# Performance work log

Hardware: AMD Instinct MI355X
Metric: run time of the kernel (lower is better)

Reference implementation:

```python
import jax, jax.numpy as jnp
import numpy as np

B, L, E, H = 4, 512, 2048, 32
S = E // H  # head_size = 64
EXTRA_MAA, EXTRA_DECAY = 32, 64
EPS = 1e-5


def setup_inputs() -> dict:
    key = jax.random.key(0)
    ks = jax.random.split(key, 24)
    rn = lambda k, shp, s=1.0: jax.random.normal(k, shp, dtype=jnp.float32) * s
    return dict(
        x=rn(ks[0], (B, L, E)),
        state=rn(ks[1], (B, 2 + S, E), 0.1),
        ln1_w=jnp.ones((E,), jnp.float32), ln1_b=jnp.zeros((E,), jnp.float32),
        ln2_w=jnp.ones((E,), jnp.float32), ln2_b=jnp.zeros((E,), jnp.float32),
        maa_x=rn(ks[2], (E,), 0.02),
        maa_w1=rn(ks[3], (E, 5 * EXTRA_MAA), 0.02),
        maa_w2=rn(ks[4], (5, EXTRA_MAA, E), 0.02),
        maa_stack=rn(ks[5], (5, E), 0.02),          # [k,w,v,r,g] time_maa vectors
        time_decay=rn(ks[6], (E,), 0.5),
        decay_w1=rn(ks[7], (E, EXTRA_DECAY), 0.02),
        decay_w2=rn(ks[8], (EXTRA_DECAY, E), 0.02),
        faaaa=rn(ks[9], (H, S), 0.1),
        Wr=rn(ks[10], (E, E), 0.02), Wk=rn(ks[11], (E, E), 0.02),
        Wv=rn(ks[12], (E, E), 0.02), Wg=rn(ks[13], (E, E), 0.02),
        Wo=rn(ks[14], (E, E), 0.02),
        gn_w=jnp.ones((E,), jnp.float32), gn_b=jnp.zeros((E,), jnp.float32),
        ffn_maa_k=rn(ks[15], (E,), 0.02), ffn_maa_r=rn(ks[16], (E,), 0.02),
        ffn_Wk=rn(ks[17], (E, E), 0.02), ffn_Wr=rn(ks[18], (E, E), 0.02),
        ffn_Wv=rn(ks[19], (E, E), 0.02),
        i=0,
    )


def _ln(x, w, b):
    m = jnp.mean(x, axis=-1, keepdims=True)
    v = jnp.mean((x - m) ** 2, axis=-1, keepdims=True)
    return (x - m) * jax.lax.rsqrt(v + EPS) * w + b


def _token_shift(xn, prev_row):
    # sx_lerp[t] = x[t-1] - x[t], with state row as x[-1]
    first = (prev_row - xn[:, 0])[:, None]
    rest = xn[:, :-1] - xn[:, 1:]
    return jnp.concatenate([first, rest], axis=1)


def reference(x, state, ln1_w, ln1_b, ln2_w, ln2_b, maa_x, maa_w1, maa_w2,
              maa_stack, time_decay, decay_w1, decay_w2, faaaa,
              Wr, Wk, Wv, Wg, Wo, gn_w, gn_b,
              ffn_maa_k, ffn_maa_r, ffn_Wk, ffn_Wr, ffn_Wv, i):
    b, l = x.shape[0], x.shape[1]
    i0 = (2 + S) * i + 0
    i1 = (2 + S) * i + 1

    # ---- time mixing (parallel) ----
    xn = _ln(x, ln1_w, ln1_b)
    sx = _token_shift(xn, state[:, i1])
    xxx = jnp.tanh((xn + sx * maa_x) @ maa_w1).reshape(b, l, 5, 1, EXTRA_MAA)
    xxx = jnp.matmul(xxx, maa_w2).reshape(b, l, 5, E)   # [B,L,5,E]
    x5 = xn[:, :, None] + sx[:, :, None] * (maa_stack + xxx)

    w = jnp.exp(-jnp.exp(time_decay + jnp.tanh(x5[:, :, 1] @ decay_w1) @ decay_w2))
    w = w.reshape(b, l, H, S)
    r = (x5[:, :, 3] @ Wr.T).reshape(b, l, H, S)
    k = (x5[:, :, 0] @ Wk.T).reshape(b, l, H, S)
    v = (x5[:, :, 2] @ Wv.T).reshape(b, l, H, S)
    g = jax.nn.silu(x5[:, :, 4] @ Wg.T)                 # [B,L,E]

    s0 = state[:, (2 + S) * i + 2:(2 + S) * (i + 1)].reshape(b, H, S, S)
    u = faaaa[None, :, :, None]                         # [1,H,S,1]

    def step(s, rkvw):
        r_t, k_t, v_t, w_t = rkvw                      # each [B,H,S]
        a = k_t[:, :, :, None] * v_t[:, :, None, :]    # [B,H,S,S] outer product
        out = jnp.einsum('bhk,bhkd->bhd', r_t, u * a + s)
        return a + w_t[:, :, :, None] * s, out

    xs = tuple(jnp.moveaxis(t, 1, 0) for t in (r, k, v, w))
    _, outs = jax.lax.scan(step, s0, xs)               # outs [L,B,H,S]
    att = jnp.moveaxis(outs, 0, 1).reshape(b, l, E)

    # group norm over each head's channels
    a4 = att.reshape(b, l, H, S)
    m = jnp.mean(a4, axis=-1, keepdims=True)
    var = jnp.mean((a4 - m) ** 2, axis=-1, keepdims=True)
    att = ((a4 - m) * jax.lax.rsqrt(var + EPS)).reshape(b, l, E) * gn_w + gn_b
    x = x + (att * g) @ Wo.T

    # ---- channel mixing (parallel) ----
    xn2 = _ln(x, ln2_w, ln2_b)
    sx2 = _token_shift(xn2, state[:, i0])
    xk = xn2 + sx2 * ffn_maa_k
    xr = xn2 + sx2 * ffn_maa_r
    rr = jax.nn.sigmoid(xr @ ffn_Wr.T)
    kk = jnp.square(jax.nn.relu(xk @ ffn_Wk.T))
    x = x + rr * (kk @ ffn_Wv.T)
    return x
```

## Files before the change

kernel.cpp:

```cpp
#include <hip/hip_runtime.h>

#define EE 2048
#define LL 512
#define BBATCH 4
#define HH 32
#define SS 64
#define EPSF 1e-5f
static constexpr size_t NEL = (size_t)BBATCH * LL * EE;

typedef __attribute__((ext_vector_type(8))) short short8;
typedef __attribute__((ext_vector_type(4))) float f32x4;

__device__ __forceinline__ unsigned short f2bf(float f) {
  union { float f; unsigned u; } x; x.f = f;
  return (unsigned short)((x.u + 0x7fffu + ((x.u >> 16) & 1u)) >> 16);
}

__device__ __forceinline__ void gload_lds16(const unsigned short* g, unsigned short* l) {
  __builtin_amdgcn_global_load_lds((const __attribute__((address_space(1))) void*)g,
                                   (__attribute__((address_space(3))) void*)l, 16, 0, 0);
}

struct CvArgs {
  const float* s[4];
  unsigned short* d[4];
};
__global__ void __launch_bounds__(256) f2bf_batch(CvArgs a, int n4) {
  int z = blockIdx.y;
  int idx = blockIdx.x * 256 + threadIdx.x;
  if (idx >= n4) return;
  float4 v = ((const float4*)a.s[z])[idx];
  ushort4 o;
  o.x = f2bf(v.x); o.y = f2bf(v.y); o.z = f2bf(v.z); o.w = f2bf(v.w);
  ((ushort4*)a.d[z])[idx] = o;
}

__global__ void __launch_bounds__(256) wprep_kernel(const float* __restrict__ w1,
                                                    const float* __restrict__ w2,
                                                    const float* __restrict__ d1,
                                                    const float* __restrict__ d2,
                                                    unsigned short* __restrict__ w1T,
                                                    unsigned short* __restrict__ w2cat,
                                                    unsigned short* __restrict__ dw1T,
                                                    unsigned short* __restrict__ dw2T) {
  const int N0 = 256 * 2048;
  const int N1 = 10240 * 160;
  const int N2 = 128 * 2048;
  const int N3 = 2048 * 128;
  int id = blockIdx.x * 256 + threadIdx.x;
  if (id < N0) {
    int n = id >> 11, k = id & 2047;
    float v = (n < 160) ? w1[(size_t)k * 160 + n] : 0.f;
    w1T[id] = f2bf(v);
    return;
  }
  id -= N0;
  if (id < N1) {
    int n = id / 160, kq = id - n * 160;
    int j = n >> 11, e = n & 2047;
    float v = ((kq >> 5) == j) ? w2[(size_t)kq * 2048 + e] : 0.f;
    w2cat[id] = f2bf(v);
    return;
  }
  id -= N1;
  if (id < N2) {
    int n = id >> 11, k = id & 2047;
    float v = (n < 64) ? d1[(size_t)k * 64 + n] : 0.f;
    dw1T[id] = f2bf(v);
    return;
  }
  id -= N2;
  if (id < N3) {
    int n = id >> 7, k = id & 127;
    float v = (k < 64) ? d2[(size_t)k * 2048 + n] : 0.f;
    dw2T[id] = f2bf(v);
  }
}

__global__ void __launch_bounds__(256) ln_kernel(const float* __restrict__ x,
                                                 const float* __restrict__ wt,
                                                 const float* __restrict__ bs,
                                                 float* __restrict__ out) {
  __shared__ float red[4];
  int tid = threadIdx.x;
  size_t base = (size_t)blockIdx.x * EE;
  int e = tid * 8;
  float4 v0 = *(const float4*)&x[base + e];
  float4 v1 = *(const float4*)&x[base + e + 4];
  float s = v0.x + v0.y + v0.z + v0.w + v1.x + v1.y + v1.z + v1.w;
#pragma unroll
  for (int off = 32; off >= 1; off >>= 1) s += __shfl_xor(s, off);
  if ((tid & 63) == 0) red[tid >> 6] = s;
  __syncthreads();
  float mean = (red[0] + red[1] + red[2] + red[3]) * (1.f / EE);
  __syncthreads();
  float d, q = 0.f;
  d = v0.x - mean; q += d * d; d = v0.y - mean; q += d * d;
  d = v0.z - mean; q += d * d; d = v0.w - mean; q += d * d;
  d = v1.x - mean; q += d * d; d = v1.y - mean; q += d * d;
  d = v1.z - mean; q += d * d; d = v1.w - mean; q += d * d;
#pragma unroll
  for (int off = 32; off >= 1; off >>= 1) q += __shfl_xor(q, off);
  if ((tid & 63) == 0) red[tid >> 6] = q;
  __syncthreads();
  float var = (red[0] + red[1] + red[2] + red[3]) * (1.f / EE);
  float rstd = rsqrtf(var + EPSF);
  float4 w0 = *(const float4*)&wt[e], w1 = *(const float4*)&wt[e + 4];
  float4 b0 = *(const float4*)&bs[e], b1 = *(const float4*)&bs[e + 4];
  float4 o0, o1;
  o0.x = (v0.x - mean) * rstd * w0.x + b0.x;
  o0.y = (v0.y - mean) * rstd * w0.y + b0.y;
  o0.z = (v0.z - mean) * rstd * w0.z + b0.z;
  o0.w = (v0.w - mean) * rstd * w0.w + b0.w;
  o1.x = (v1.x - mean) * rstd * w1.x + b1.x;
  o1.y = (v1.y - mean) * rstd * w1.y + b1.y;
  o1.z = (v1.z - mean) * rstd * w1.z + b1.z;
  o1.w = (v1.w - mean) * rstd * w1.w + b1.w;
  *(float4*)&out[base + e] = o0;
  *(float4*)&out[base + e + 4] = o1;
}

__global__ void __launch_bounds__(256) shift_kernel(const float* __restrict__ xn,
                                                    const float* __restrict__ state,
                                                    const int* __restrict__ ip,
                                                    const float* __restrict__ maa_x,
                                                    unsigned short* __restrict__ xxm,
                                                    float* __restrict__ sx) {
  int tok = blockIdx.x;
  int b = tok >> 9, t = tok & 511;
  int tid = threadIdx.x;
  const float* cur = xn + (size_t)tok * EE;
  const float* prev = (t == 0)
      ? (state + ((size_t)b * (2 + SS) + (size_t)(2 + SS) * (*ip) + 1) * EE)
      : (cur - EE);
  int e = tid * 8;
#pragma unroll
  for (int half = 0; half < 2; ++half) {
    int eh = e + half * 4;
    float4 c = *(const float4*)&cur[eh];
    float4 p = *(const float4*)&prev[eh];
    float4 mx = *(const float4*)&maa_x[eh];
    float4 sv;
    sv.x = p.x - c.x; sv.y = p.y - c.y; sv.z = p.z - c.z; sv.w = p.w - c.w;
    *(float4*)&sx[(size_t)tok * EE + eh] = sv;
    ushort4 xo;
    xo.x = f2bf(c.x + sv.x * mx.x);
    xo.y = f2bf(c.y + sv.y * mx.y);
    xo.z = f2bf(c.z + sv.z * mx.z);
    xo.w = f2bf(c.w + sv.w * mx.w);
    *(ushort4*)&xxm[(size_t)tok * EE + eh] = xo;
  }
}

template <int BM, int BN, int BK>
__device__ __forceinline__ void gemm_core(const unsigned short* __restrict__ A, int lda,
                                          const unsigned short* __restrict__ W, int ldw,
                                          int K, int NB, unsigned short* As, unsigned short* Bs,
                                          f32x4 (&acc)[BM / 32][BN / 32], int& m0o, int& n0o) {
  constexpr int FM = BM / 32, FN = BN / 32;
  constexpr int GPR = BK / 8;
  constexpr int LA = BM * GPR / 256;
  constexpr int LB = BN * GPR / 256;
  int nwg = gridDim.x, bid = blockIdx.x;
  int qd = nwg >> 3;
  int wg = (bid & 7) * qd + (bid >> 3);
  int bm = wg / NB, bn = wg - bm * NB;
  int tid = threadIdx.x;
  int wave = tid >> 6, lane = tid & 63;
  int wm = wave >> 1, wn = wave & 1;
  const unsigned short* Abase = A + (size_t)bm * BM * lda;
  const unsigned short* Bbase = W + (size_t)bn * BN * ldw;
  for (int k0 = 0; k0 < K; k0 += BK) {
    __syncthreads();
#pragma unroll
    for (int r = 0; r < LA; ++r) {
      int g = r * 256 + tid;
      int row = g / GPR, p = g & (GPR - 1);
      int lg = p ^ (row & (GPR - 1));
      gload_lds16(Abase + (size_t)row * lda + k0 + lg * 8, &As[g * 8]);
    }
#pragma unroll
    for (int r = 0; r < LB; ++r) {
      int g = r * 256 + tid;
      int row = g / GPR, p = g & (GPR - 1);
      int lg = p ^ (row & (GPR - 1));
      gload_lds16(Bbase + (size_t)row * ldw + k0 + lg * 8, &Bs[g * 8]);
    }
    __syncthreads();
    int q = lane >> 4;
    int rA = wm * (BM / 2) + (lane & 15);
    int rB = wn * (BN / 2) + (lane & 15);
    int xrA = rA & (GPR - 1), xrB = rB & (GPR - 1);
#pragma unroll
    for (int ks = 0; ks < BK / 32; ++ks) {
      short8 av[FM], bv[FN];
#pragma unroll
      for (int f = 0; f < FM; f++) {
        int p = (ks * 4 + q) ^ xrA;
        av[f] = *(const short8*)&As[(rA + f * 16) * BK + p * 8];
      }
#pragma unroll
      for (int f = 0; f < FN; f++) {
        int p = (ks * 4 + q) ^ xrB;
        bv[f] = *(const short8*)&Bs[(rB + f * 16) * BK + p * 8];
      }
#pragma unroll
      for (int fm = 0; fm < FM; fm++)
#pragma unroll
        for (int fn = 0; fn < FN; fn++)
          acc[fm][fn] =
              __builtin_amdgcn_mfma_f32_16x16x32_bf16(av[fm], bv[fn], acc[fm][fn], 0, 0, 0);
    }
  }
  m0o = bm * BM + wm * (BM / 2);
  n0o = bn * BN + wn * (BN / 2);
}

template <int FM, int FN, typename F>
__device__ __forceinline__ void epi_loop(f32x4 (&acc)[FM][FN], int m0, int n0, F f) {
  int lane = threadIdx.x & 63;
  int rl = (lane >> 4) * 4, cl = lane & 15;
#pragma unroll
  for (int fm = 0; fm < FM; fm++)
#pragma unroll
    for (int fn = 0; fn < FN; fn++)
#pragma unroll
      for (int q = 0; q < 4; q++)
        f(m0 + fm * 16 + rl + q, n0 + fn * 16 + cl, acc[fm][fn][q]);
}

template <int MODE, int BM, int BN, int BK>
__global__ void __launch_bounds__(256) gemm_bt(const unsigned short* __restrict__ A, int lda,
                                               const unsigned short* __restrict__ W, int ldw,
                                               int K, int NB, void* __restrict__ Cout, int ldc,
                                               const float* __restrict__ p1,
                                               const float* __restrict__ p2,
                                               const float* __restrict__ p3) {
  __shared__ __align__(16) unsigned short As[BM * BK];
  __shared__ __align__(16) unsigned short Bs[BN * BK];
  f32x4 acc[BM / 32][BN / 32] = {};
  int m0, n0;
  gemm_core<BM, BN, BK>(A, lda, W, ldw, K, NB, As, Bs, acc, m0, n0);
  epi_loop(acc, m0, n0, [&](int m, int n, float val) {
    size_t o = (size_t)m * ldc + n;
    if constexpr (MODE == 2) {
      ((float*)Cout)[o] = p1[o] + val;
    } else if constexpr (MODE == 3) {
      ((float*)Cout)[o] = p1[o] + val * (1.f / (1.f + expf(-p2[o])));
    } else if constexpr (MODE == 5) {
      ((unsigned short*)Cout)[o] = f2bf(tanhf(val));
    } else if constexpr (MODE == 6) {
      ((float*)Cout)[o] = expf(-expf(p1[n] + val));
    } else {
      int j = n >> 11, e = n & 2047;
      size_t oe = (size_t)m * EE + e;
      float xv = p1[oe];
      float sv = p2[oe];
      float st = p3[(size_t)j * EE + e];
      ((unsigned short*)Cout)[(size_t)j * NEL + oe] = f2bf(xv + sv * (st + val));
    }
  });
}

struct Proj4Args {
  const unsigned short* A[4];
  const unsigned short* W[4];
  float* C[4];
};
__global__ void __launch_bounds__(256) gemm_proj4(Proj4Args args) {
  __shared__ __align__(16) unsigned short As[128 * 64];
  __shared__ __align__(16) unsigned short Bs[128 * 64];
  int z = blockIdx.y;
  f32x4 acc[4][4] = {};
  int m0, n0;
  gemm_core<128, 128, 64>(args.A[z], EE, args.W[z], EE, EE, 16, As, Bs, acc, m0, n0);
  float* C = args.C[z];
  bool silu = (z == 3);
  epi_loop(acc, m0, n0, [&](int m, int n, float val) {
    size_t o = (size_t)m * EE + n;
    C[o] = silu ? (val / (1.f + expf(-val))) : val;
  });
}

__global__ void __launch_bounds__(256) gemm_ffn2(const unsigned short* A0,
                                                 const unsigned short* A1,
                                                 const unsigned short* W0,
                                                 const unsigned short* W1, float* C0,
                                                 unsigned short* C1) {
  __shared__ __align__(16) unsigned short As[128 * 64];
  __shared__ __align__(16) unsigned short Bs[128 * 64];
  int z = blockIdx.y;
  f32x4 acc[4][4] = {};
  int m0, n0;
  gemm_core<128, 128, 64>(z ? A1 : A0, EE, z ? W1 : W0, EE, EE, 16, As, Bs, acc, m0, n0);
  epi_loop(acc, m0, n0, [&](int m, int n, float val) {
    size_t o = (size_t)m * EE + n;
    if (z == 0) {
      C0[o] = val;
    } else {
      float rv = fmaxf(val, 0.f);
      C1[o] = f2bf(rv * rv);
    }
  });
}

__global__ void __launch_bounds__(512) scan_kernel(const float* __restrict__ r,
                                                   const float* __restrict__ k,
                                                   const float* __restrict__ v,
                                                   const float* __restrict__ w,
                                                   const float* __restrict__ state,
                                                   const float* __restrict__ faaaa,
                                                   const int* __restrict__ ip,
                                                   float* __restrict__ att) {
  __shared__ float bR[2][8][32], bK[2][8][32], bW[2][8][32];
  __shared__ float bV[2][8][64];
  __shared__ float part[8][8][64];
  int blk = blockIdx.x;
  int bh = blk >> 1, kh = blk & 1;
  int b = bh >> 5, h = bh & 31;
  int tid = threadIdx.x, wv = tid >> 6, lane = tid & 63;
  int klocal = wv * 4;
  int k0w = kh * 32 + klocal;
  int ii = *ip;
  const float* sb = state + ((size_t)b * (2 + SS) + (size_t)(2 + SS) * ii + 2) * EE;
  float s_[4], u_[4];
#pragma unroll
  for (int q = 0; q < 4; ++q) {
    int kk_ = k0w + q;
    s_[q] = sb[(size_t)(2 * h + (kk_ >> 5)) * EE + (kk_ & 31) * 64 + lane];
    u_[q] = faaaa[h * 64 + kk_];
  }
  size_t base = (size_t)b * LL * EE + (size_t)h * 64;
  int c = tid;
  bool ld = c < 320;
  int lt = c / 40, r40 = c - lt * 40;
  int la = (r40 < 24) ? (r40 >> 3) : 3;
  int lcG = (r40 < 24) ? (kh * 32 + (r40 & 7) * 4) : ((r40 - 24) * 4);
  int lcL = (r40 < 24) ? ((r40 & 7) * 4) : ((r40 - 24) * 4);
  const float* lsrc = nullptr;
  if (ld) {
    const float* arr = (la == 0) ? r : (la == 1) ? k : (la == 2) ? w : v;
    lsrc = arr + base + (size_t)lt * EE + lcG;
    float4 v0 = *(const float4*)lsrc;
    if (la == 0) *(float4*)&bR[0][lt][lcL] = v0;
    else if (la == 1) *(float4*)&bK[0][lt][lcL] = v0;
    else if (la == 2) *(float4*)&bW[0][lt][lcL] = v0;
    else *(float4*)&bV[0][lt][lcL] = v0;
  }
  __syncthreads();
  for (int g = 0; g < 64; ++g) {
    int cb = g & 1;
    float4 nv;
    if (ld && g < 63) nv = *(const float4*)(lsrc + (size_t)(g + 1) * 8 * EE);
#pragma unroll
    for (int t = 0; t < 8; ++t) {
      float vv = bV[cb][t][lane];
      float acc = 0.f;
#pragma unroll
      for (int q = 0; q < 4; ++q) {
        float rk = bR[cb][t][klocal + q];
        float kk2 = bK[cb][t][klocal + q];
        float wk = bW[cb][t][klocal + q];
        float a = kk2 * vv;
        acc = fmaf(rk, fmaf(u_[q], a, s_[q]), acc);
        s_[q] = fmaf(wk, s_[q], a);
      }
      part[t][wv][lane] = acc;
    }
    if (ld && g < 63) {
      int nb = cb ^ 1;
      if (la == 0) *(float4*)&bR[nb][lt][lcL] = nv;
      else if (la == 1) *(float4*)&bK[nb][lt][lcL] = nv;
      else if (la == 2) *(float4*)&bW[nb][lt][lcL] = nv;
      else *(float4*)&bV[nb][lt][lcL] = nv;
    }
    __syncthreads();
    {
      int t = tid >> 6, d = tid & 63;
      float tot = part[t][0][d] + part[t][1][d] + part[t][2][d] + part[t][3][d] +
                  part[t][4][d] + part[t][5][d] + part[t][6][d] + part[t][7][d];
      atomicAdd(&att[base + (size_t)(g * 8 + t) * EE + d], tot);
    }
    __syncthreads();
  }
}

__global__ void __launch_bounds__(256) gn_gate_kernel(const float* __restrict__ att,
                                                      const float* __restrict__ g,
                                                      const float* __restrict__ gnw,
                                                      const float* __restrict__ gnb,
                                                      unsigned short* __restrict__ attg) {
  int tok = blockIdx.x, tid = threadIdx.x;
  int h = tid >> 3, j = tid & 7;
  size_t base = (size_t)tok * EE + h * 64 + j * 8;
  int e = h * 64 + j * 8;
  float4 a0 = *(const float4*)&att[base];
  float4 a1 = *(const float4*)&att[base + 4];
  float s = a0.x + a0.y + a0.z + a0.w + a1.x + a1.y + a1.z + a1.w;
  s += __shfl_xor(s, 1); s += __shfl_xor(s, 2); s += __shfl_xor(s, 4);
  float mean = s * (1.f / 64.f);
  float d, q = 0.f;
  d = a0.x - mean; q += d * d; d = a0.y - mean; q += d * d;
  d = a0.z - mean; q += d * d; d = a0.w - mean; q += d * d;
  d = a1.x - mean; q += d * d; d = a1.y - mean; q += d * d;
  d = a1.z - mean; q += d * d; d = a1.w - mean; q += d * d;
  q += __shfl_xor(q, 1); q += __shfl_xor(q, 2); q += __shfl_xor(q, 4);
  float rstd = rsqrtf(q * (1.f / 64.f) + EPSF);
  float4 w0 = *(const float4*)&gnw[e], w1 = *(const float4*)&gnw[e + 4];
  float4 b0 = *(const float4*)&gnb[e], b1 = *(const float4*)&gnb[e + 4];
  float4 g0 = *(const float4*)&g[base], g1 = *(const float4*)&g[base + 4];
  ushort4 o0, o1;
  o0.x = f2bf(((a0.x - mean) * rstd * w0.x + b0.x) * g0.x);
  o0.y = f2bf(((a0.y - mean) * rstd * w0.y + b0.y) * g0.y);
  o0.z = f2bf(((a0.z - mean) * rstd * w0.z + b0.z) * g0.z);
  o0.w = f2bf(((a0.w - mean) * rstd * w0.w + b0.w) * g0.w);
  o1.x = f2bf(((a1.x - mean) * rstd * w1.x + b1.x) * g1.x);
  o1.y = f2bf(((a1.y - mean) * rstd * w1.y + b1.y) * g1.y);
  o1.z = f2bf(((a1.z - mean) * rstd * w1.z + b1.z) * g1.z);
  o1.w = f2bf(((a1.w - mean) * rstd * w1.w + b1.w) * g1.w);
  *(ushort4*)&attg[base] = o0;
  *(ushort4*)&attg[base + 4] = o1;
}

__global__ void __launch_bounds__(256) ffn_shift_kernel(const float* __restrict__ xn2,
                                                        const float* __restrict__ state,
                                                        const int* __restrict__ ip,
                                                        const float* __restrict__ mk,
                                                        const float* __restrict__ mr,
                                                        unsigned short* __restrict__ xkb,
                                                        unsigned short* __restrict__ xrb) {
  size_t i4 = (size_t)blockIdx.x * 256 + threadIdx.x;
  size_t e0 = i4 * 4;
  if (e0 >= NEL) return;
  int tok = (int)(e0 >> 11);
  int c = (int)(e0 & 2047);
  int b = tok >> 9, t = tok & 511;
  float4 cur = *(const float4*)&xn2[e0];
  float4 prev;
  if (t == 0) {
    int ii = *ip;
    prev = *(const float4*)&state[((size_t)b * (2 + SS) + (size_t)(2 + SS) * ii + 0) * EE + c];
  } else {
    prev = *(const float4*)&xn2[e0 - EE];
  }
  float4 k4 = *(const float4*)&mk[c];
  float4 r4 = *(const float4*)&mr[c];
  ushort4 ko, ro;
  ko.x = f2bf(cur.x + (prev.x - cur.x) * k4.x);
  ko.y = f2bf(cur.y + (prev.y - cur.y) * k4.y);
  ko.z = f2bf(cur.z + (prev.z - cur.z) * k4.z);
  ko.w = f2bf(cur.w + (prev.w - cur.w) * k4.w);
  ro.x = f2bf(cur.x + (prev.x - cur.x) * r4.x);
  ro.y = f2bf(cur.y + (prev.y - cur.y) * r4.y);
  ro.z = f2bf(cur.z + (prev.z - cur.z) * r4.z);
  ro.w = f2bf(cur.w + (prev.w - cur.w) * r4.w);
  *(ushort4*)&xkb[e0] = ko;
  *(ushort4*)&xrb[e0] = ro;
}

extern "C" void kernel_launch(void* const* d_in, const int* in_sizes, int n_in,
                              void* d_out, int out_size, void* d_ws, size_t ws_size,
                              hipStream_t stream) {
  const float* x = (const float*)d_in[0];
  const float* state = (const float*)d_in[1];
  const float* ln1_w = (const float*)d_in[2];
  const float* ln1_b = (const float*)d_in[3];
  const float* ln2_w = (const float*)d_in[4];
  const float* ln2_b = (const float*)d_in[5];
  const float* maa_x = (const float*)d_in[6];
  const float* maa_w1 = (const float*)d_in[7];
  const float* maa_w2 = (const float*)d_in[8];
  const float* maa_stack = (const float*)d_in[9];
  const float* time_decay = (const float*)d_in[10];
  const float* decay_w1 = (const float*)d_in[11];
  const float* decay_w2 = (const float*)d_in[12];
  const float* faaaa = (const float*)d_in[13];
  const float* Wr = (const float*)d_in[14];
  const float* Wk = (const float*)d_in[15];
  const float* Wv = (const float*)d_in[16];
  const float* Wg = (const float*)d_in[17];
  const float* Wo = (const float*)d_in[18];
  const float* gn_w = (const float*)d_in[19];
  const float* gn_b = (const float*)d_in[20];
  const float* ffn_maa_k = (const float*)d_in[21];
  const float* ffn_maa_r = (const float*)d_in[22];
  const float* fWk = (const float*)d_in[23];
  const float* fWr = (const float*)d_in[24];
  const float* fWv = (const float*)d_in[25];
  const int* ip = (const int*)d_in[26];

  char* ws = (char*)d_ws;
  const size_t MB1 = 1024 * 1024;
  unsigned short* WB0 = (unsigned short*)ws;
  unsigned short* WB1 = (unsigned short*)(ws + 8 * MB1);
  float* xn = (float*)(ws + 16 * MB1);
  unsigned short* x5b = (unsigned short*)(ws + 32 * MB1);
  float* wbuf = (float*)(ws + 72 * MB1);
  float* rbuf = (float*)(ws + 88 * MB1);
  float* kbuf = (float*)(ws + 104 * MB1);
  float* vbuf = (float*)(ws + 120 * MB1);
  float* gbuf = (float*)(ws + 136 * MB1);
  char* smalls = ws + 152 * MB1;
  unsigned short* th = (unsigned short*)smalls;
  unsigned short* w1T = (unsigned short*)(smalls + 1 * MB1);
  unsigned short* w2cat = (unsigned short*)(smalls + 2 * MB1);
  unsigned short* dw1T = (unsigned short*)(smalls + 5376 * 1024);
  unsigned short* dw2T = (unsigned short*)(smalls + 5888 * 1024);
  unsigned short* dt = (unsigned short*)(smalls + 6400 * 1024);

  unsigned short* xxm = (unsigned short*)wbuf;
  float* sx = gbuf;
  float* att = xn;
  unsigned short* WB2 = (unsigned short*)xn;
  unsigned short* WB3 = WB2 + NEL;
  unsigned short* attg = x5b;
  float* xn2 = rbuf;
  unsigned short* xkb = x5b + 1 * NEL;
  unsigned short* xrb = x5b + 2 * NEL;
  unsigned short* kkb = x5b + 3 * NEL;
  unsigned short* fWkB = x5b + 4 * NEL;
  unsigned short* fWvB = (unsigned short*)kbuf;
  float* rrraw = wbuf;

  const int thr = 256;
  const int nconv = (int)(NEL / 4);

  ln_kernel<<<BBATCH * LL, thr, 0, stream>>>(x, ln1_w, ln1_b, xn);
  shift_kernel<<<BBATCH * LL, thr, 0, stream>>>(xn, state, ip, maa_x, xxm, sx);
  wprep_kernel<<<10496, thr, 0, stream>>>(maa_w1, maa_w2, decay_w1, decay_w2, w1T, w2cat,
                                          dw1T, dw2T);
  gemm_bt<5, 64, 64, 64><<<128, thr, 0, stream>>>(xxm, 2048, w1T, 2048, 2048, 4, th, 256,
                                                  nullptr, nullptr, nullptr);
  gemm_bt<7, 128, 128, 32><<<1280, thr, 0, stream>>>(th, 256, w2cat, 160, 160, 80, x5b, 0,
                                                     xn, sx, maa_stack);
  gemm_bt<5, 64, 64, 64><<<64, thr, 0, stream>>>(x5b + 1 * NEL, 2048, dw1T, 2048, 2048, 2,
                                                 dt, 128, nullptr, nullptr, nullptr);
  gemm_bt<6, 128, 128, 64><<<256, thr, 0, stream>>>(dt, 128, dw2T, 128, 128, 16, wbuf, 2048,
                                                    time_decay, nullptr, nullptr);
  {
    CvArgs ca;
    ca.s[0] = Wk; ca.d[0] = WB0;
    ca.s[1] = Wv; ca.d[1] = WB1;
    ca.s[2] = Wr; ca.d[2] = WB2;
    ca.s[3] = Wg; ca.d[3] = WB3;
    f2bf_batch<<<dim3(4096, 4), thr, 0, stream>>>(ca, nconv);
  }
  {
    Proj4Args pa;
    pa.A[0] = x5b + 0 * NEL; pa.W[0] = WB0; pa.C[0] = kbuf;
    pa.A[1] = x5b + 2 * NEL; pa.W[1] = WB1; pa.C[1] = vbuf;
    pa.A[2] = x5b + 3 * NEL; pa.W[2] = WB2; pa.C[2] = rbuf;
    pa.A[3] = x5b + 4 * NEL; pa.W[3] = WB3; pa.C[3] = gbuf;
    gemm_proj4<<<dim3(256, 4), thr, 0, stream>>>(pa);
  }
  {
    CvArgs cb;
    cb.s[0] = Wo; cb.d[0] = WB0;
    cb.s[1] = fWr; cb.d[1] = WB1;
    cb.s[2] = fWk; cb.d[2] = fWkB;
    cb.s[3] = fWk; cb.d[3] = fWkB;
    f2bf_batch<<<dim3(4096, 3), thr, 0, stream>>>(cb, nconv);
  }
  (void)hipMemsetAsync(att, 0, NEL * sizeof(float), stream);
  scan_kernel<<<256, 512, 0, stream>>>(rbuf, kbuf, vbuf, wbuf, state, faaaa, ip, att);
  {
    CvArgs cc;
    cc.s[0] = fWv; cc.d[0] = fWvB;
    cc.s[1] = fWv; cc.d[1] = fWvB;
    cc.s[2] = fWv; cc.d[2] = fWvB;
    cc.s[3] = fWv; cc.d[3] = fWvB;
    f2bf_batch<<<dim3(4096, 1), thr, 0, stream>>>(cc, nconv);
  }
  gn_gate_kernel<<<BBATCH * LL, thr, 0, stream>>>(att, gbuf, gn_w, gn_b, attg);
  gemm_bt<2, 128, 64, 64><<<512, thr, 0, stream>>>(attg, 2048, WB0, 2048, 2048, 32,
                                                   (float*)d_out, 2048, x, nullptr, nullptr);
  ln_kernel<<<BBATCH * LL, thr, 0, stream>>>((const float*)d_out, ln2_w, ln2_b, xn2);
  ffn_shift_kernel<<<4096, thr, 0, stream>>>(xn2, state, ip, ffn_maa_k, ffn_maa_r, xkb, xrb);
  gemm_ffn2<<<dim3(256, 2), thr, 0, stream>>>(xrb, xkb, WB1, fWkB, rrraw, kkb);
  gemm_bt<3, 128, 64, 64><<<512, thr, 0, stream>>>(kkb, 2048, fWvB, 2048, 2048, 32,
                                                   (float*)d_out, 2048, (const float*)d_out,
                                                   rrraw, nullptr);
}
```

Baseline: 480.1 us.

## Double-buffer GEMM LDS tiles with async prefetch and fuse layernorm with token shift

The shared GEMM core now keeps two LDS tile buffers and issues global-to-LDS loads two K-steps ahead, waiting on vmcnt instead of synchronising on every tile. It also raises wave priority around the MFMA block. Separately, layernorm and token-shift are fused into one kernel per side that recomputes the previous row's norm, which removes the intermediate xn2 round trip and one launch. The cost is doubled LDS per block, which may lower occupancy, plus redundant reductions for the previous row and some wasted wrap-around prefetches at the tail.

```diff
diff --git a/kernel.cpp b/kernel.cpp
--- a/kernel.cpp
+++ b/kernel.cpp
@@ -19,6 +19,14 @@
 __device__ __forceinline__ void gload_lds16(const unsigned short* g, unsigned short* l) {
   __builtin_amdgcn_global_load_lds((const __attribute__((address_space(1))) void*)g,
                                    (__attribute__((address_space(3))) void*)l, 16, 0, 0);
+}
+
+template <int N>
+__device__ __forceinline__ void wait_vmcnt_n() {
+  if constexpr (N == 4) asm volatile("s_waitcnt vmcnt(4)" ::: "memory");
+  else if constexpr (N == 6) asm volatile("s_waitcnt vmcnt(6)" ::: "memory");
+  else if constexpr (N == 8) asm volatile("s_waitcnt vmcnt(8)" ::: "memory");
+  else asm volatile("s_waitcnt vmcnt(0)" ::: "memory");
 }
 
 struct CvArgs {
@@ -77,90 +85,132 @@
   }
 }
 
-__global__ void __launch_bounds__(256) ln_kernel(const float* __restrict__ x,
-                                                 const float* __restrict__ wt,
-                                                 const float* __restrict__ bs,
-                                                 float* __restrict__ out) {
-  __shared__ float red[4];
-  int tid = threadIdx.x;
-  size_t base = (size_t)blockIdx.x * EE;
-  int e = tid * 8;
-  float4 v0 = *(const float4*)&x[base + e];
-  float4 v1 = *(const float4*)&x[base + e + 4];
-  float s = v0.x + v0.y + v0.z + v0.w + v1.x + v1.y + v1.z + v1.w;
-#pragma unroll
-  for (int off = 32; off >= 1; off >>= 1) s += __shfl_xor(s, off);
-  if ((tid & 63) == 0) red[tid >> 6] = s;
-  __syncthreads();
-  float mean = (red[0] + red[1] + red[2] + red[3]) * (1.f / EE);
-  __syncthreads();
-  float d, q = 0.f;
-  d = v0.x - mean; q += d * d; d = v0.y - mean; q += d * d;
-  d = v0.z - mean; q += d * d; d = v0.w - mean; q += d * d;
-  d = v1.x - mean; q += d * d; d = v1.y - mean; q += d * d;
-  d = v1.z - mean; q += d * d; d = v1.w - mean; q += d * d;
-#pragma unroll
-  for (int off = 32; off >= 1; off >>= 1) q += __shfl_xor(q, off);
-  if ((tid & 63) == 0) red[tid >> 6] = q;
-  __syncthreads();
-  float var = (red[0] + red[1] + red[2] + red[3]) * (1.f / EE);
-  float rstd = rsqrtf(var + EPSF);
-  float4 w0 = *(const float4*)&wt[e], w1 = *(const float4*)&wt[e + 4];
-  float4 b0 = *(const float4*)&bs[e], b1 = *(const float4*)&bs[e + 4];
-  float4 o0, o1;
-  o0.x = (v0.x - mean) * rstd * w0.x + b0.x;
-  o0.y = (v0.y - mean) * rstd * w0.y + b0.y;
-  o0.z = (v0.z - mean) * rstd * w0.z + b0.z;
-  o0.w = (v0.w - mean) * rstd * w0.w + b0.w;
-  o1.x = (v1.x - mean) * rstd * w1.x + b1.x;
-  o1.y = (v1.y - mean) * rstd * w1.y + b1.y;
-  o1.z = (v1.z - mean) * rstd * w1.z + b1.z;
-  o1.w = (v1.w - mean) * rstd * w1.w + b1.w;
-  *(float4*)&out[base + e] = o0;
-  *(float4*)&out[base + e + 4] = o1;
-}
-
-__global__ void __launch_bounds__(256) shift_kernel(const float* __restrict__ xn,
-                                                    const float* __restrict__ state,
-                                                    const int* __restrict__ ip,
-                                                    const float* __restrict__ maa_x,
-                                                    unsigned short* __restrict__ xxm,
-                                                    float* __restrict__ sx) {
+template <int SIDE>
+__global__ void __launch_bounds__(256) ln_shift_kernel(
+    const float* __restrict__ x, const float* __restrict__ state, const int* __restrict__ ip,
+    const float* __restrict__ lnw, const float* __restrict__ lnb,
+    const float* __restrict__ mA, const float* __restrict__ mB,
+    float* __restrict__ xn_out, unsigned short* __restrict__ o1,
+    float* __restrict__ sx_out, unsigned short* __restrict__ o2) {
+  __shared__ float red[8];
   int tok = blockIdx.x;
   int b = tok >> 9, t = tok & 511;
   int tid = threadIdx.x;
-  const float* cur = xn + (size_t)tok * EE;
-  const float* prev = (t == 0)
-      ? (state + ((size_t)b * (2 + SS) + (size_t)(2 + SS) * (*ip) + 1) * EE)
-      : (cur - EE);
   int e = tid * 8;
-#pragma unroll
-  for (int half = 0; half < 2; ++half) {
-    int eh = e + half * 4;
-    float4 c = *(const float4*)&cur[eh];
-    float4 p = *(const float4*)&prev[eh];
-    float4 mx = *(const float4*)&maa_x[eh];
-    float4 sv;
-    sv.x = p.x - c.x; sv.y = p.y - c.y; sv.z = p.z - c.z; sv.w = p.w - c.w;
-    *(float4*)&sx[(size_t)tok * EE + eh] = sv;
-    ushort4 xo;
-    xo.x = f2bf(c.x + sv.x * mx.x);
-    xo.y = f2bf(c.y + sv.y * mx.y);
-    xo.z = f2bf(c.z + sv.z * mx.z);
-    xo.w = f2bf(c.w + sv.w * mx.w);
-    *(ushort4*)&xxm[(size_t)tok * EE + eh] = xo;
+  size_t base = (size_t)tok * EE;
+  float c[8], p[8];
+  *(float4*)&c[0] = *(const float4*)&x[base + e];
+  *(float4*)&c[4] = *(const float4*)&x[base + e + 4];
+  bool hasp = (t != 0);
+  if (hasp) {
+    *(float4*)&p[0] = *(const float4*)&x[base - EE + e];
+    *(float4*)&p[4] = *(const float4*)&x[base - EE + e + 4];
+  } else {
+    const float* srow = state + ((size_t)b * (2 + SS) + (size_t)(2 + SS) * (*ip) +
+                                 (SIDE == 0 ? 1 : 0)) * EE;
+    *(float4*)&p[0] = *(const float4*)&srow[e];
+    *(float4*)&p[4] = *(const float4*)&srow[e + 4];
+  }
+  float sc = 0.f, sp = 0.f;
+#pragma unroll
+  for (int j = 0; j < 8; ++j) { sc += c[j]; sp += p[j]; }
+#pragma unroll
+  for (int off = 32; off >= 1; off >>= 1) {
+    sc += __shfl_xor(sc, off);
+    sp += __shfl_xor(sp, off);
+  }
+  if ((tid & 63) == 0) { red[tid >> 6] = sc; red[4 + (tid >> 6)] = sp; }
+  __syncthreads();
+  float mc = (red[0] + red[1] + red[2] + red[3]) * (1.f / EE);
+  float mp = (red[4] + red[5] + red[6] + red[7]) * (1.f / EE);
+  __syncthreads();
+  float qc = 0.f, qp = 0.f;
+#pragma unroll
+  for (int j = 0; j < 8; ++j) {
+    float dc = c[j] - mc, dp = p[j] - mp;
+    qc += dc * dc; qp += dp * dp;
+  }
+#pragma unroll
+  for (int off = 32; off >= 1; off >>= 1) {
+    qc += __shfl_xor(qc, off);
+    qp += __shfl_xor(qp, off);
+  }
+  if ((tid & 63) == 0) { red[tid >> 6] = qc; red[4 + (tid >> 6)] = qp; }
+  __syncthreads();
+  float rc = rsqrtf((red[0] + red[1] + red[2] + red[3]) * (1.f / EE) + EPSF);
+  float rp = rsqrtf((red[4] + red[5] + red[6] + red[7]) * (1.f / EE) + EPSF);
+  float wv[8], bv[8], av[8], bv2[8];
+  *(float4*)&wv[0] = *(const float4*)&lnw[e];
+  *(float4*)&wv[4] = *(const float4*)&lnw[e + 4];
+  *(float4*)&bv[0] = *(const float4*)&lnb[e];
+  *(float4*)&bv[4] = *(const float4*)&lnb[e + 4];
+  *(float4*)&av[0] = *(const float4*)&mA[e];
+  *(float4*)&av[4] = *(const float4*)&mA[e + 4];
+  if (SIDE == 1) {
+    *(float4*)&bv2[0] = *(const float4*)&mB[e];
+    *(float4*)&bv2[4] = *(const float4*)&mB[e + 4];
+  }
+  float cn[8], sxv[8];
+#pragma unroll
+  for (int j = 0; j < 8; ++j) {
+    float cnj = (c[j] - mc) * rc * wv[j] + bv[j];
+    float pnj = hasp ? ((p[j] - mp) * rp * wv[j] + bv[j]) : p[j];
+    cn[j] = cnj;
+    sxv[j] = pnj - cnj;
+  }
+  if constexpr (SIDE == 0) {
+    *(float4*)&xn_out[base + e] = *(float4*)&cn[0];
+    *(float4*)&xn_out[base + e + 4] = *(float4*)&cn[4];
+    *(float4*)&sx_out[base + e] = *(float4*)&sxv[0];
+    *(float4*)&sx_out[base + e + 4] = *(float4*)&sxv[4];
+    ushort4 xo0, xo1;
+    xo0.x = f2bf(cn[0] + sxv[0] * av[0]); xo0.y = f2bf(cn[1] + sxv[1] * av[1]);
+    xo0.z = f2bf(cn[2] + sxv[2] * av[2]); xo0.w = f2bf(cn[3] + sxv[3] * av[3]);
+    xo1.x = f2bf(cn[4] + sxv[4] * av[4]); xo1.y = f2bf(cn[5] + sxv[5] * av[5]);
+    xo1.z = f2bf(cn[6] + sxv[6] * av[6]); xo1.w = f2bf(cn[7] + sxv[7] * av[7]);
+    *(ushort4*)&o1[base + e] = xo0;
+    *(ushort4*)&o1[base + e + 4] = xo1;
+  } else {
+    ushort4 k0, k1, r0, r1;
+    k0.x = f2bf(cn[0] + sxv[0] * av[0]); k0.y = f2bf(cn[1] + sxv[1] * av[1]);
+    k0.z = f2bf(cn[2] + sxv[2] * av[2]); k0.w = f2bf(cn[3] + sxv[3] * av[3]);
+    k1.x = f2bf(cn[4] + sxv[4] * av[4]); k1.y = f2bf(cn[5] + sxv[5] * av[5]);
+    k1.z = f2bf(cn[6] + sxv[6] * av[6]); k1.w = f2bf(cn[7] + sxv[7] * av[7]);
+    r0.x = f2bf(cn[0] + sxv[0] * bv2[0]); r0.y = f2bf(cn[1] + sxv[1] * bv2[1]);
+    r0.z = f2bf(cn[2] + sxv[2] * bv2[2]); r0.w = f2bf(cn[3] + sxv[3] * bv2[3]);
+    r1.x = f2bf(cn[4] + sxv[4] * bv2[4]); r1.y = f2bf(cn[5] + sxv[5] * bv2[5]);
+    r1.z = f2bf(cn[6] + sxv[6] * bv2[6]); r1.w = f2bf(cn[7] + sxv[7] * bv2[7]);
+    *(ushort4*)&o1[base + e] = k0;
+    *(ushort4*)&o1[base + e + 4] = k1;
+    *(ushort4*)&o2[base + e] = r0;
+    *(ushort4*)&o2[base + e + 4] = r1;
+  }
+}
+
+template <int ROWS, int BK>
+__device__ __forceinline__ void stage_mat(const unsigned short* __restrict__ base, int ld,
+                                          int k0, unsigned short* dst) {
+  constexpr int GPR = BK / 8;
+  constexpr int L = ROWS * GPR / 256;
+  int tid = threadIdx.x;
+#pragma unroll
+  for (int r = 0; r < L; ++r) {
+    int g = r * 256 + tid;
+    int row = g / GPR, p = g & (GPR - 1);
+    int lg = p ^ (row & (GPR - 1));
+    gload_lds16(base + (size_t)row * ld + k0 + lg * 8, &dst[g * 8]);
   }
 }
 
 template <int BM, int BN, int BK>
 __device__ __forceinline__ void gemm_core(const unsigned short* __restrict__ A, int lda,
                                           const unsigned short* __restrict__ W, int ldw,
-                                          int K, int NB, unsigned short* As, unsigned short* Bs,
+                                          int K, int NB, unsigned short* AsAll,
+                                          unsigned short* BsAll,
                                           f32x4 (&acc)[BM / 32][BN / 32], int& m0o, int& n0o) {
-  constexpr int FM = BM / 32, FN = BN / 32;
+  constexpr int FM = BM / 32, FN = BN / 32, KS = BK / 32;
   constexpr int GPR = BK / 8;
-  constexpr int LA = BM * GPR / 256;
-  constexpr int LB = BN * GPR / 256;
+  constexpr int NLD = (BM + BN) * GPR / 256;
   int nwg = gridDim.x, bid = blockIdx.x;
   int qd = nwg >> 3;
   int wg = (bid & 7) * qd + (bid >> 3);
@@ -170,47 +220,55 @@
   int wm = wave >> 1, wn = wave & 1;
   const unsigned short* Abase = A + (size_t)bm * BM * lda;
   const unsigned short* Bbase = W + (size_t)bn * BN * ldw;
-  for (int k0 = 0; k0 < K; k0 += BK) {
-    __syncthreads();
-#pragma unroll
-    for (int r = 0; r < LA; ++r) {
-      int g = r * 256 + tid;
-      int row = g / GPR, p = g & (GPR - 1);
-      int lg = p ^ (row & (GPR - 1));
-      gload_lds16(Abase + (size_t)row * lda + k0 + lg * 8, &As[g * 8]);
-    }
-#pragma unroll
-    for (int r = 0; r < LB; ++r) {
-      int g = r * 256 + tid;
-      int row = g / GPR, p = g & (GPR - 1);
-      int lg = p ^ (row & (GPR - 1));
-      gload_lds16(Bbase + (size_t)row * ldw + k0 + lg * 8, &Bs[g * 8]);
-    }
-    __syncthreads();
-    int q = lane >> 4;
-    int rA = wm * (BM / 2) + (lane & 15);
-    int rB = wn * (BN / 2) + (lane & 15);
-    int xrA = rA & (GPR - 1), xrB = rB & (GPR - 1);
-#pragma unroll
-    for (int ks = 0; ks < BK / 32; ++ks) {
-      short8 av[FM], bv[FN];
+  const int T = K / BK;
+  stage_mat<BM, BK>(Abase, lda, 0, AsAll);
+  stage_mat<BN, BK>(Bbase, ldw, 0, BsAll);
+  {
+    int k1 = (T > 1) ? BK : 0;
+    stage_mat<BM, BK>(Abase, lda, k1, AsAll + BM * BK);
+    stage_mat<BN, BK>(Bbase, ldw, k1, BsAll + BN * BK);
+  }
+  int q = lane >> 4;
+  int rA = wm * (BM / 2) + (lane & 15);
+  int rB = wn * (BN / 2) + (lane & 15);
+  int xrA = rA & (GPR - 1), xrB = rB & (GPR - 1);
+  for (int t = 0; t < T; ++t) {
+    unsigned short* As = AsAll + (t & 1) * (BM * BK);
+    unsigned short* Bs = BsAll + (t & 1) * (BN * BK);
+    wait_vmcnt_n<NLD>();
+    __builtin_amdgcn_s_barrier();
+    __builtin_amdgcn_sched_barrier(0);
+    short8 av[KS][FM], bv[KS][FN];
+#pragma unroll
+    for (int ks = 0; ks < KS; ++ks) {
 #pragma unroll
       for (int f = 0; f < FM; f++) {
         int p = (ks * 4 + q) ^ xrA;
-        av[f] = *(const short8*)&As[(rA + f * 16) * BK + p * 8];
+        av[ks][f] = *(const short8*)&As[(rA + f * 16) * BK + p * 8];
       }
 #pragma unroll
       for (int f = 0; f < FN; f++) {
         int p = (ks * 4 + q) ^ xrB;
-        bv[f] = *(const short8*)&Bs[(rB + f * 16) * BK + p * 8];
+        bv[ks][f] = *(const short8*)&Bs[(rB + f * 16) * BK + p * 8];
       }
+    }
+    asm volatile("s_waitcnt lgkmcnt(0)" ::: "memory");
+    __builtin_amdgcn_sched_barrier(0);
+    __builtin_amdgcn_s_barrier();
+    int tn = t + 2;
+    if (tn >= T) tn -= T;
+    stage_mat<BM, BK>(Abase, lda, tn * BK, As);
+    stage_mat<BN, BK>(Bbase, ldw, tn * BK, Bs);
+    __builtin_amdgcn_s_setprio(1);
+#pragma unroll
+    for (int ks = 0; ks < KS; ++ks)
 #pragma unroll
       for (int fm = 0; fm < FM; fm++)
 #pragma unroll
         for (int fn = 0; fn < FN; fn++)
-          acc[fm][fn] =
-              __builtin_amdgcn_mfma_f32_16x16x32_bf16(av[fm], bv[fn], acc[fm][fn], 0, 0, 0);
-    }
+          acc[fm][fn] = __builtin_amdgcn_mfma_f32_16x16x32_bf16(av[ks][fm], bv[ks][fn],
+                                                                acc[fm][fn], 0, 0, 0);
+    __builtin_amdgcn_s_setprio(0);
   }
   m0o = bm * BM + wm * (BM / 2);
   n0o = bn * BN + wn * (BN / 2);
@@ -236,8 +294,8 @@
                                                const float* __restrict__ p1,
                                                const float* __restrict__ p2,
                                                const float* __restrict__ p3) {
-  __shared__ __align__(16) unsigned short As[BM * BK];
-  __shared__ __align__(16) unsigned short Bs[BN * BK];
+  __shared__ __align__(16) unsigned short As[2 * BM * BK];
+  __shared__ __align__(16) unsigned short Bs[2 * BN * BK];
   f32x4 acc[BM / 32][BN / 32] = {};
   int m0, n0;
   gemm_core<BM, BN, BK>(A, lda, W, ldw, K, NB, As, Bs, acc, m0, n0);
@@ -268,8 +326,8 @@
   float* C[4];
 };
 __global__ void __launch_bounds__(256) gemm_proj4(Proj4Args args) {
-  __shared__ __align__(16) unsigned short As[128 * 64];
-  __shared__ __align__(16) unsigned short Bs[128 * 64];
+  __shared__ __align__(16) unsigned short As[2 * 128 * 64];
+  __shared__ __align__(16) unsigned short Bs[2 * 128 * 64];
   int z = blockIdx.y;
   f32x4 acc[4][4] = {};
   int m0, n0;
@@ -287,8 +345,8 @@
                                                  const unsigned short* W0,
                                                  const unsigned short* W1, float* C0,
                                                  unsigned short* C1) {
-  __shared__ __align__(16) unsigned short As[128 * 64];
-  __shared__ __align__(16) unsigned short Bs[128 * 64];
+  __shared__ __align__(16) unsigned short As[2 * 128 * 64];
+  __shared__ __align__(16) unsigned short Bs[2 * 128 * 64];
   int z = blockIdx.y;
   f32x4 acc[4][4] = {};
   int m0, n0;
@@ -422,42 +480,6 @@
   *(ushort4*)&attg[base + 4] = o1;
 }
 
-__global__ void __launch_bounds__(256) ffn_shift_kernel(const float* __restrict__ xn2,
-                                                        const float* __restrict__ state,
-                                                        const int* __restrict__ ip,
-                                                        const float* __restrict__ mk,
-                                                        const float* __restrict__ mr,
-                                                        unsigned short* __restrict__ xkb,
-                                                        unsigned short* __restrict__ xrb) {
-  size_t i4 = (size_t)blockIdx.x * 256 + threadIdx.x;
-  size_t e0 = i4 * 4;
-  if (e0 >= NEL) return;
-  int tok = (int)(e0 >> 11);
-  int c = (int)(e0 & 2047);
-  int b = tok >> 9, t = tok & 511;
-  float4 cur = *(const float4*)&xn2[e0];
-  float4 prev;
-  if (t == 0) {
-    int ii = *ip;
-    prev = *(const float4*)&state[((size_t)b * (2 + SS) + (size_t)(2 + SS) * ii + 0) * EE + c];
-  } else {
-    prev = *(const float4*)&xn2[e0 - EE];
-  }
-  float4 k4 = *(const float4*)&mk[c];
-  float4 r4 = *(const float4*)&mr[c];
-  ushort4 ko, ro;
-  ko.x = f2bf(cur.x + (prev.x - cur.x) * k4.x);
-  ko.y = f2bf(cur.y + (prev.y - cur.y) * k4.y);
-  ko.z = f2bf(cur.z + (prev.z - cur.z) * k4.z);
-  ko.w = f2bf(cur.w + (prev.w - cur.w) * k4.w);
-  ro.x = f2bf(cur.x + (prev.x - cur.x) * r4.x);
-  ro.y = f2bf(cur.y + (prev.y - cur.y) * r4.y);
-  ro.z = f2bf(cur.z + (prev.z - cur.z) * r4.z);
-  ro.w = f2bf(cur.w + (prev.w - cur.w) * r4.w);
-  *(ushort4*)&xkb[e0] = ko;
-  *(ushort4*)&xrb[e0] = ro;
-}
-
 extern "C" void kernel_launch(void* const* d_in, const int* in_sizes, int n_in,
                               void* d_out, int out_size, void* d_ws, size_t ws_size,
                               hipStream_t stream) {
@@ -514,7 +536,6 @@
   unsigned short* WB2 = (unsigned short*)xn;
   unsigned short* WB3 = WB2 + NEL;
   unsigned short* attg = x5b;
-  float* xn2 = rbuf;
   unsigned short* xkb = x5b + 1 * NEL;
   unsigned short* xrb = x5b + 2 * NEL;
   unsigned short* kkb = x5b + 3 * NEL;
@@ -525,8 +546,8 @@
   const int thr = 256;
   const int nconv = (int)(NEL / 4);
 
-  ln_kernel<<<BBATCH * LL, thr, 0, stream>>>(x, ln1_w, ln1_b, xn);
-  shift_kernel<<<BBATCH * LL, thr, 0, stream>>>(xn, state, ip, maa_x, xxm, sx);
+  ln_shift_kernel<0><<<BBATCH * LL, thr, 0, stream>>>(x, state, ip, ln1_w, ln1_b, maa_x,
+                                                      nullptr, xn, xxm, sx, nullptr);
   wprep_kernel<<<10496, thr, 0, stream>>>(maa_w1, maa_w2, decay_w1, decay_w2, w1T, w2cat,
                                           dw1T, dw2T);
   gemm_bt<5, 64, 64, 64><<<128, thr, 0, stream>>>(xxm, 2048, w1T, 2048, 2048, 4, th, 256,
@@ -574,8 +595,9 @@
   gn_gate_kernel<<<BBATCH * LL, thr, 0, stream>>>(att, gbuf, gn_w, gn_b, attg);
   gemm_bt<2, 128, 64, 64><<<512, thr, 0, stream>>>(attg, 2048, WB0, 2048, 2048, 32,
                                                    (float*)d_out, 2048, x, nullptr, nullptr);
-  ln_kernel<<<BBATCH * LL, thr, 0, stream>>>((const float*)d_out, ln2_w, ln2_b, xn2);
-  ffn_shift_kernel<<<4096, thr, 0, stream>>>(xn2, state, ip, ffn_maa_k, ffn_maa_r, xkb, xrb);
+  ln_shift_kernel<1><<<BBATCH * LL, thr, 0, stream>>>((const float*)d_out, state, ip, ln2_w,
+                                                      ln2_b, ffn_maa_k, ffn_maa_r, nullptr,
+                                                      xkb, nullptr, xrb);
   gemm_ffn2<<<dim3(256, 2), thr, 0, stream>>>(xrb, xkb, WB1, fWkB, rrraw, kkb);
   gemm_bt<3, 128, 64, 64><<<512, thr, 0, stream>>>(kkb, 2048, fWvB, 2048, 2048, 32,
                                                    (float*)d_out, 2048, (const float*)d_out,
```

After: 435.0 us. 9.4% less time.
